# Optimization experiments

Hardware: AMD Instinct MI355X
Metric: run time of the kernel (lower is better)

## Reference

```python
import jax, jax.numpy as jnp
import numpy as np

B, S, E, NH = 1, 2048, 1024, 8
DH = E // NH
EPS_BACKEND = 1e-6  # eps in parallel_stabilized_simple
EPS_NORM = 1e-5     # MultiHeadLayerNorm (group_norm) eps


def setup_inputs() -> dict:
    key = jax.random.key(0)
    ks = jax.random.split(key, 8)
    q = jax.random.normal(ks[0], (B, S, E), jnp.float32)
    k = jax.random.normal(ks[1], (B, S, E), jnp.float32)
    v = jax.random.normal(ks[2], (B, S, E), jnp.float32)
    # gate Linear params: weight (NH, 3E), bias (NH). Small scale so gates are
    # in a realistic regime (fgate bias ~ linspace(3,6) per the torch init).
    igate_w = jax.random.normal(ks[3], (NH, 3 * E), jnp.float32) * 0.02
    igate_b = jax.random.normal(ks[4], (NH,), jnp.float32) * 0.1
    fgate_w = jax.random.normal(ks[5], (NH, 3 * E), jnp.float32) * 0.02
    fgate_b = jnp.linspace(3.0, 6.0, NH).astype(jnp.float32)
    norm_w = 1.0 + 0.1 * jax.random.normal(ks[6], (E,), jnp.float32)
    return dict(q=q, k=k, v=v, igate_w=igate_w, igate_b=igate_b,
                fgate_w=fgate_w, fgate_b=fgate_b, norm_w=norm_w)


def reference(q, k, v, igate_w, igate_b, fgate_w, fgate_b, norm_w):
    Bq, Sq, Eq = q.shape
    nh = igate_w.shape[0]
    dh = Eq // nh
    # gate pre-activations from concatenated q,k,v
    gate_in = jnp.concatenate([q, k, v], axis=-1)             # (B,S,3E)
    ig = jnp.transpose(gate_in @ igate_w.T + igate_b, (0, 2, 1))  # (B,NH,S)
    fg = jnp.transpose(gate_in @ fgate_w.T + fgate_b, (0, 2, 1))  # (B,NH,S)
    # split heads: (B,NH,S,DH)
    qh = q.reshape(Bq, Sq, nh, dh).transpose(0, 2, 1, 3)
    kh = k.reshape(Bq, Sq, nh, dh).transpose(0, 2, 1, 3)
    vh = v.reshape(Bq, Sq, nh, dh).transpose(0, 2, 1, 3)
    # cumulative log forget gates; decay matrix entry (t,s) = cs[t]-cs[s]
    log_f_cum = jnp.cumsum(jax.nn.log_sigmoid(fg), axis=-1)   # (B,NH,S)
    log_fg_mat = log_f_cum[:, :, :, None] - log_f_cum[:, :, None, :]  # (B,NH,S,S)
    ltr = jnp.tril(jnp.ones((Sq, Sq), dtype=bool))            # causal mask
    log_D = jnp.where(ltr, log_fg_mat + ig[:, :, None, :], -jnp.inf)
    # row-wise stabilizer
    max_log_D = jnp.max(log_D, axis=-1, keepdims=True)        # (B,NH,S,1)
    D = jnp.exp(log_D - max_log_D)
    qk = jnp.einsum('bhsd,bhtd->bhst', qh, kh) / jnp.sqrt(jnp.float32(dh))
    C = qk * D
    normalizer = jnp.maximum(jnp.abs(jnp.sum(C, axis=-1, keepdims=True)),
                             jnp.exp(-max_log_D))
    h = jnp.einsum('bhst,bhtd->bhsd', C / (normalizer + EPS_BACKEND), vh)
    # MultiHeadLayerNorm == group_norm with NH groups over (NH*DH), per-channel weight
    mean = jnp.mean(h, axis=-1, keepdims=True)
    var = jnp.var(h, axis=-1, keepdims=True)
    h_norm = (h - mean) / jnp.sqrt(var + EPS_NORM)
    h_norm = h_norm * norm_w.reshape(nh, dh)[None, :, None, :]
    return h_norm.transpose(0, 2, 1, 3).reshape(Bq, Sq, Eq)
```

## Files before the change

### kernel.cpp

```cpp
#include <hip/hip_runtime.h>
#include <hip/hip_bf16.h>
#include <math.h>

#define S_LEN 2048
#define E_DIM 1024
#define NHEAD 8
#define DH 128
#define E3 3072

typedef short bf16x8 __attribute__((ext_vector_type(8)));
typedef short bf16x4 __attribute__((ext_vector_type(4)));
typedef float f32x4 __attribute__((ext_vector_type(4)));
typedef float f32x16 __attribute__((ext_vector_type(16)));

#define MFMA3216(a,b,c) __builtin_amdgcn_mfma_f32_32x32x16_bf16(a,b,c,0,0,0)
#define Z16 {0.f,0.f,0.f,0.f,0.f,0.f,0.f,0.f,0.f,0.f,0.f,0.f,0.f,0.f,0.f,0.f}
#define CROW(r) (((r)&3) + 8*((r)>>2))

__device__ __forceinline__ unsigned short f2bf(float f){
  union{float f; unsigned u;} x; x.f = f;
  unsigned r = x.u + 0x7FFF + ((x.u>>16)&1);
  return (unsigned short)(r>>16);
}

__device__ __forceinline__ unsigned cvtpk(float lo, float hi){
  unsigned r;
  asm("v_cvt_pk_bf16_f32 %0, %1, %2" : "=v"(r) : "v"(lo), "v"(hi));
  return r;
}

__device__ __forceinline__ float logsigf(float x){
  return fminf(x, 0.f) - log1pf(expf(-fabsf(x)));
}

typedef const __attribute__((address_space(1))) unsigned int* gas1_t;
typedef __attribute__((address_space(3))) unsigned int* las3_t;
__device__ __forceinline__ void stage16(const ushort* g, ushort* l){
  __builtin_amdgcn_global_load_lds((gas1_t)(const void*)g, (las3_t)(void*)l, 16, 0, 0);
}

__global__ __launch_bounds__(256) void gates_qk(
    const float* __restrict__ q, const float* __restrict__ k, const float* __restrict__ v,
    const float* __restrict__ igw, const float* __restrict__ igb,
    const float* __restrict__ fgw, const float* __restrict__ fgb,
    float* __restrict__ ig_out, float* __restrict__ lsf_out,
    ushort* __restrict__ qbo, ushort* __restrict__ kbo, ushort* __restrict__ vto){
  const int t0 = blockIdx.x*4;
  const int tid = threadIdx.x;
  const int lane = tid & 63, wv = tid >> 6;
  float acc[64];
  #pragma unroll
  for (int a=0;a<64;++a) acc[a]=0.f;
  const float sc = 0.08838834764831845f;
  #pragma unroll
  for (int step=0; step<3; ++step){
    const float* src = (step==0)? q : ((step==1)? k : v);
    float4 in4[4];
    #pragma unroll
    for (int r=0;r<4;++r) in4[r] = ((const float4*)src)[(size_t)(t0+r)*256 + tid];
    if (step==0){
      #pragma unroll
      for (int r=0;r<4;++r){
        ushort4 o; o.x=f2bf(in4[r].x*sc); o.y=f2bf(in4[r].y*sc);
        o.z=f2bf(in4[r].z*sc); o.w=f2bf(in4[r].w*sc);
        ((ushort4*)qbo)[(size_t)(t0+r)*256 + tid] = o;
      }
    } else if (step==1){
      #pragma unroll
      for (int r=0;r<4;++r){
        ushort4 o; o.x=f2bf(in4[r].x); o.y=f2bf(in4[r].y);
        o.z=f2bf(in4[r].z); o.w=f2bf(in4[r].w);
        ((ushort4*)kbo)[(size_t)(t0+r)*256 + tid] = o;
      }
    } else {
      #pragma unroll
      for (int c=0;c<4;++c){
        ushort4 ov;
        ov.x = f2bf(((const float*)&in4[0])[c]);
        ov.y = f2bf(((const float*)&in4[1])[c]);
        ov.z = f2bf(((const float*)&in4[2])[c]);
        ov.w = f2bf(((const float*)&in4[3])[c]);
        *(ushort4*)(vto + (size_t)(tid*4+c)*S_LEN + t0) = ov;
      }
    }
    const int wj = step*256 + tid;
    #pragma unroll
    for (int o=0;o<8;++o){
      float4 wI = ((const float4*)igw)[o*768 + wj];
      float4 wF = ((const float4*)fgw)[o*768 + wj];
      #pragma unroll
      for (int r=0;r<4;++r){
        acc[o*4+r]    = fmaf(in4[r].x, wI.x, acc[o*4+r]);
        acc[o*4+r]    = fmaf(in4[r].y, wI.y, acc[o*4+r]);
        acc[o*4+r]    = fmaf(in4[r].z, wI.z, acc[o*4+r]);
        acc[o*4+r]    = fmaf(in4[r].w, wI.w, acc[o*4+r]);
        acc[32+o*4+r] = fmaf(in4[r].x, wF.x, acc[32+o*4+r]);
        acc[32+o*4+r] = fmaf(in4[r].y, wF.y, acc[32+o*4+r]);
        acc[32+o*4+r] = fmaf(in4[r].z, wF.z, acc[32+o*4+r]);
        acc[32+o*4+r] = fmaf(in4[r].w, wF.w, acc[32+o*4+r]);
      }
    }
  }
  int cnt = 32;
  #pragma unroll
  for (int s=0; s<6; ++s){
    const bool hib = (lane >> s) & 1;
    #pragma unroll
    for (int a=0; a<32; ++a){
      if (a < cnt){
        float sent = hib ? acc[a] : acc[a+cnt];
        float got = __shfl_xor(sent, 1<<s, 64);
        acc[a] = (hib ? acc[a+cnt] : acc[a]) + got;
      }
    }
    cnt >>= 1;
  }
  __shared__ float red[4][64];
  red[wv][lane] = acc[0];
  __syncthreads();
  if (tid < 64){
    float tot = red[0][tid]+red[1][tid]+red[2][tid]+red[3][tid];
    int a = (int)(__brev((unsigned)tid) >> 26);
    int f = a >> 5, o = (a>>2)&7, r = a&3;
    int t = t0 + r;
    if (f==0) ig_out[o*S_LEN + t] = tot + igb[o];
    else      lsf_out[o*S_LEN + t] = logsigf(tot + fgb[o]);
  }
}

__global__ __launch_bounds__(256) void scan_kernel(
    const float* __restrict__ ig, const float* __restrict__ lsf,
    float* __restrict__ cs_out, float* __restrict__ M_out, float* __restrict__ m_out){
  const int h = blockIdx.x;
  const int tid = threadIdx.x;
  __shared__ float tt[256];
  const int base = tid*8;
  const float* src = lsf + h*S_LEN;
  float loc[8]; float tot = 0.f;
  #pragma unroll
  for (int i=0;i<8;++i){ tot += src[base+i]; loc[i]=tot; }
  tt[tid]=tot; __syncthreads();
  for (int off=1; off<256; off<<=1){
    float add = (tid>=off)? tt[tid-off] : 0.f;
    __syncthreads();
    tt[tid] += add;
    __syncthreads();
  }
  const float excl = tt[tid] - tot;
  float csv[8];
  #pragma unroll
  for (int i=0;i<8;++i){ csv[i] = excl + loc[i]; cs_out[h*S_LEN+base+i]=csv[i]; }
  const float* igp = ig + h*S_LEN;
  float mloc[8], mval[8]; float mtot = -INFINITY;
  #pragma unroll
  for (int i=0;i<8;++i){
    float m = igp[base+i] - csv[i];
    mval[i] = m;
    mtot = fmaxf(mtot, m);
    mloc[i] = mtot;
  }
  __syncthreads();
  tt[tid]=mtot; __syncthreads();
  for (int off=1; off<256; off<<=1){
    float add = (tid>=off)? tt[tid-off] : -INFINITY;
    __syncthreads();
    tt[tid] = fmaxf(tt[tid], add);
    __syncthreads();
  }
  const float exclm = (tid>0)? tt[tid-1] : -INFINITY;
  #pragma unroll
  for (int i=0;i<8;++i){
    M_out[h*S_LEN+base+i] = fmaxf(exclm, mloc[i]);
    m_out[h*S_LEN+base+i] = mval[i];
  }
}

__global__ __launch_bounds__(256, 2) void mlstm_mfma6(
    const ushort* __restrict__ qb, const ushort* __restrict__ kb,
    const ushort* __restrict__ vt,
    const float* __restrict__ csb, const float* __restrict__ Mxb,
    const float* __restrict__ mbb,
    const float* __restrict__ nw, float* __restrict__ out){
  const int h = blockIdx.x;
  const int qt = 63 - blockIdx.y;
  const int tid = threadIdx.x, l = tid & 63;
  const int sq = tid >> 6;
  const int l31 = l & 31, l15 = l & 15, hi = l >> 5;

  __shared__ __align__(16) float UNI[4*32*132];
  __shared__ float MB[128];
  __shared__ float rsL[4][32];
  ushort* Kb = (ushort*)UNI;
  ushort* Vb = Kb + 16384;
  float*  Part = UNI;

  const int hS = h*S_LEN;
  const ushort* kbh = kb + h*DH;
  const ushort* vth = vt + (size_t)h*DH*S_LEN;
  const float*  mh  = mbb + hS;
  const int t0 = qt*32;
  const int NT = (t0 + 31)/128 + 1;
  const int tgq = t0 + l31;
  const float Mq = Mxb[hS + tgq];

  bf16x8 qf0,qf1,qf2,qf3,qf4,qf5,qf6,qf7;
  { const ushort* qs = qb + (size_t)tgq*E_DIM + h*DH + hi*8;
    qf0 = *(const bf16x8*)(qs+0);   qf1 = *(const bf16x8*)(qs+16);
    qf2 = *(const bf16x8*)(qs+32);  qf3 = *(const bf16x8*)(qs+48);
    qf4 = *(const bf16x8*)(qs+64);  qf5 = *(const bf16x8*)(qs+80);
    qf6 = *(const bf16x8*)(qs+96);  qf7 = *(const bf16x8*)(qs+112); }

  f32x16 a0 = Z16, a1 = Z16, a2 = Z16, a3 = Z16;
  float rsq = 0.f;

#define STAGE6(ktv) {                                                        \
    _Pragma("unroll")                                                        \
    for (int i_=0;i_<8;++i_){                                                \
      const int L_ = tid + i_*256; const int row_ = L_>>4, pc_ = L_&15;      \
      stage16(kbh + (size_t)((ktv)*128+row_)*E_DIM + ((pc_^(row_&15))<<3),   \
              Kb + (size_t)L_*8); }                                          \
    _Pragma("unroll")                                                        \
    for (int i_=0;i_<8;++i_){                                                \
      const int L_ = tid + i_*256; const int d_ = L_>>4, pc_ = L_&15;        \
      stage16(vth + (size_t)d_*S_LEN + (ktv)*128 + ((pc_^(d_&15))<<3),       \
              Vb + (size_t)L_*8); }                                          \
    if (tid < 32)                                                            \
      stage16((const ushort*)(mh + (ktv)*128) + tid*8,                       \
              (ushort*)MB + tid*8); }

#define LV6(dt, cs) (*(const bf16x8*)(Vb + (size_t)((dt)*32+l31)*128 + (((cs)^l15)<<3)))

  for (int kt=0; kt<NT; ++kt){
    if (kt) __syncthreads();
    STAGE6(kt);
    __syncthreads();

    const ushort* kbase = Kb + (size_t)(sq*32 + l31)*128;
    f32x16 cc = Z16;
    { bf16x8 ka;
      ka = *(const bf16x8*)(kbase + (((0*2+hi)^l15)<<3)); cc = MFMA3216(ka, qf0, cc);
      ka = *(const bf16x8*)(kbase + (((1*2+hi)^l15)<<3)); cc = MFMA3216(ka, qf1, cc);
      ka = *(const bf16x8*)(kbase + (((2*2+hi)^l15)<<3)); cc = MFMA3216(ka, qf2, cc);
      ka = *(const bf16x8*)(kbase + (((3*2+hi)^l15)<<3)); cc = MFMA3216(ka, qf3, cc);
      ka = *(const bf16x8*)(kbase + (((4*2+hi)^l15)<<3)); cc = MFMA3216(ka, qf4, cc);
      ka = *(const bf16x8*)(kbase + (((5*2+hi)^l15)<<3)); cc = MFMA3216(ka, qf5, cc);
      ka = *(const bf16x8*)(kbase + (((6*2+hi)^l15)<<3)); cc = MFMA3216(ka, qf6, cc);
      ka = *(const bf16x8*)(kbase + (((7*2+hi)^l15)<<3)); cc = MFMA3216(ka, qf7, cc); }

    bf16x8 fE, fO;
    {
      const int sb_ = kt*128 + sq*32 + 4*hi;
      const f32x4 mA_ = *(const f32x4*)&MB[sq*32 +  0 + 4*hi];
      const f32x4 mB_ = *(const f32x4*)&MB[sq*32 +  8 + 4*hi];
      const f32x4 mC_ = *(const f32x4*)&MB[sq*32 + 16 + 4*hi];
      const f32x4 mD_ = *(const f32x4*)&MB[sq*32 + 24 + 4*hi];
      float p0  = (sb_+0  <= tgq) ? cc[0] *__expf(mA_[0]-Mq) : 0.f;
      float p1  = (sb_+1  <= tgq) ? cc[1] *__expf(mA_[1]-Mq) : 0.f;
      float p2  = (sb_+2  <= tgq) ? cc[2] *__expf(mA_[2]-Mq) : 0.f;
      float p3  = (sb_+3  <= tgq) ? cc[3] *__expf(mA_[3]-Mq) : 0.f;
      float p4  = (sb_+8  <= tgq) ? cc[4] *__expf(mB_[0]-Mq) : 0.f;
      float p5  = (sb_+9  <= tgq) ? cc[5] *__expf(mB_[1]-Mq) : 0.f;
      float p6  = (sb_+10 <= tgq) ? cc[6] *__expf(mB_[2]-Mq) : 0.f;
      float p7  = (sb_+11 <= tgq) ? cc[7] *__expf(mB_[3]-Mq) : 0.f;
      float p8  = (sb_+16 <= tgq) ? cc[8] *__expf(mC_[0]-Mq) : 0.f;
      float p9  = (sb_+17 <= tgq) ? cc[9] *__expf(mC_[1]-Mq) : 0.f;
      float p10 = (sb_+18 <= tgq) ? cc[10]*__expf(mC_[2]-Mq) : 0.f;
      float p11 = (sb_+19 <= tgq) ? cc[11]*__expf(mC_[3]-Mq) : 0.f;
      float p12 = (sb_+24 <= tgq) ? cc[12]*__expf(mD_[0]-Mq) : 0.f;
      float p13 = (sb_+25 <= tgq) ? cc[13]*__expf(mD_[1]-Mq) : 0.f;
      float p14 = (sb_+26 <= tgq) ? cc[14]*__expf(mD_[2]-Mq) : 0.f;
      float p15 = (sb_+27 <= tgq) ? cc[15]*__expf(mD_[3]-Mq) : 0.f;
      rsq += ((p0+p1)+(p2+p3))+((p4+p5)+(p6+p7))
           + ((p8+p9)+(p10+p11))+((p12+p13)+(p14+p15));
      unsigned A0_=cvtpk(p0,p1),  A1_=cvtpk(p2,p3);
      unsigned B0_=cvtpk(p4,p5),  B1_=cvtpk(p6,p7);
      unsigned C0_=cvtpk(p8,p9),  C1_=cvtpk(p10,p11);
      unsigned D0_=cvtpk(p12,p13),D1_=cvtpk(p14,p15);
      unsigned A0x_=(unsigned)__shfl_xor((int)A0_,32,64);
      unsigned B0x_=(unsigned)__shfl_xor((int)B0_,32,64);
      unsigned A1x_=(unsigned)__shfl_xor((int)A1_,32,64);
      unsigned B1x_=(unsigned)__shfl_xor((int)B1_,32,64);
      unsigned C0x_=(unsigned)__shfl_xor((int)C0_,32,64);
      unsigned D0x_=(unsigned)__shfl_xor((int)D0_,32,64);
      unsigned C1x_=(unsigned)__shfl_xor((int)C1_,32,64);
      unsigned D1x_=(unsigned)__shfl_xor((int)D1_,32,64);
      { unsigned* u_ = (unsigned*)&fE;
        u_[0] = hi ? B0x_ : A0_;  u_[1] = hi ? B1x_ : A1_;
        u_[2] = hi ? B0_  : A0x_; u_[3] = hi ? B1_  : A1x_; }
      { unsigned* u_ = (unsigned*)&fO;
        u_[0] = hi ? D0x_ : C0_;  u_[1] = hi ? D1x_ : C1_;
        u_[2] = hi ? D0_  : C0x_; u_[3] = hi ? D1_  : C1x_; }
    }

    a0 = MFMA3216(fE, LV6(0, sq*4 + 0 + hi), a0);
    a1 = MFMA3216(fE, LV6(1, sq*4 + 0 + hi), a1);
    a2 = MFMA3216(fE, LV6(2, sq*4 + 0 + hi), a2);
    a3 = MFMA3216(fE, LV6(3, sq*4 + 0 + hi), a3);
    a0 = MFMA3216(fO, LV6(0, sq*4 + 2 + hi), a0);
    a1 = MFMA3216(fO, LV6(1, sq*4 + 2 + hi), a1);
    a2 = MFMA3216(fO, LV6(2, sq*4 + 2 + hi), a2);
    a3 = MFMA3216(fO, LV6(3, sq*4 + 2 + hi), a3);
  }

  __syncthreads();
  #pragma unroll
  for (int r=0;r<16;++r){
    const int qrow = CROW(r) + 4*hi;
    float* pr = Part + (size_t)(sq*32 + qrow)*132 + l31;
    pr[0]  = a0[r];
    pr[32] = a1[r];
    pr[64] = a2[r];
    pr[96] = a3[r];
  }
  rsq += __shfl_xor(rsq, 32, 64);
  if (l < 32) rsL[sq][l31] = rsq;
  __syncthreads();

  {
    const int q = tid >> 3, dg = tid & 7;
    f32x4 os0={0.f,0.f,0.f,0.f}, os1=os0, os2=os0, os3=os0;
    #pragma unroll
    for (int w2=0; w2<4; ++w2){
      const float* pb = Part + (size_t)(w2*32 + q)*132 + dg*16;
      os0 += *(const f32x4*)(pb+0);
      os1 += *(const f32x4*)(pb+4);
      os2 += *(const f32x4*)(pb+8);
      os3 += *(const f32x4*)(pb+12);
    }
    const float rstot = rsL[0][q]+rsL[1][q]+rsL[2][q]+rsL[3][q];
    const int tq = t0 + q;
    const float en = __expf(-(csb[hS+tq] + Mxb[hS+tq]));
    const float iv = 1.f/(fmaxf(fabsf(rstot), en) + 1e-6f);
    f32x4 h0, h1, h2, h3;
    h0[0]=os0[0]*iv; h0[1]=os0[1]*iv; h0[2]=os0[2]*iv; h0[3]=os0[3]*iv;
    h1[0]=os1[0]*iv; h1[1]=os1[1]*iv; h1[2]=os1[2]*iv; h1[3]=os1[3]*iv;
    h2[0]=os2[0]*iv; h2[1]=os2[1]*iv; h2[2]=os2[2]*iv; h2[3]=os2[3]*iv;
    h3[0]=os3[0]*iv; h3[1]=os3[1]*iv; h3[2]=os3[2]*iv; h3[3]=os3[3]*iv;
    float s1 = (h0[0]+h0[1]+h0[2]+h0[3]) + (h1[0]+h1[1]+h1[2]+h1[3])
             + (h2[0]+h2[1]+h2[2]+h2[3]) + (h3[0]+h3[1]+h3[2]+h3[3]);
    float s2 = (h0[0]*h0[0]+h0[1]*h0[1]+h0[2]*h0[2]+h0[3]*h0[3])
             + (h1[0]*h1[0]+h1[1]*h1[1]+h1[2]*h1[2]+h1[3]*h1[3])
             + (h2[0]*h2[0]+h2[1]*h2[1]+h2[2]*h2[2]+h2[3]*h2[3])
             + (h3[0]*h3[0]+h3[1]*h3[1]+h3[2]*h3[2]+h3[3]*h3[3]);
    s1 += __shfl_xor(s1, 1, 64);  s2 += __shfl_xor(s2, 1, 64);
    s1 += __shfl_xor(s1, 2, 64);  s2 += __shfl_xor(s2, 2, 64);
    s1 += __shfl_xor(s1, 4, 64);  s2 += __shfl_xor(s2, 4, 64);
    const float mean = s1*(1.f/128.f);
    const float var  = s2*(1.f/128.f) - mean*mean;
    const float rstd = rsqrtf(var + 1e-5f);
    const float* nb = nw + h*DH + dg*16;
    const f32x4 n0 = *(const f32x4*)(nb+0);
    const f32x4 n1 = *(const f32x4*)(nb+4);
    const f32x4 n2 = *(const f32x4*)(nb+8);
    const f32x4 n3 = *(const f32x4*)(nb+12);
    float* ob = out + (size_t)tq*E_DIM + h*DH + dg*16;
    f32x4 o0v, o1v, o2v, o3v;
    o0v[0]=(h0[0]-mean)*rstd*n0[0]; o0v[1]=(h0[1]-mean)*rstd*n0[1];
    o0v[2]=(h0[2]-mean)*rstd*n0[2]; o0v[3]=(h0[3]-mean)*rstd*n0[3];
    o1v[0]=(h1[0]-mean)*rstd*n1[0]; o1v[1]=(h1[1]-mean)*rstd*n1[1];
    o1v[2]=(h1[2]-mean)*rstd*n1[2]; o1v[3]=(h1[3]-mean)*rstd*n1[3];
    o2v[0]=(h2[0]-mean)*rstd*n2[0]; o2v[1]=(h2[1]-mean)*rstd*n2[1];
    o2v[2]=(h2[2]-mean)*rstd*n2[2]; o2v[3]=(h2[3]-mean)*rstd*n2[3];
    o3v[0]=(h3[0]-mean)*rstd*n3[0]; o3v[1]=(h3[1]-mean)*rstd*n3[1];
    o3v[2]=(h3[2]-mean)*rstd*n3[2]; o3v[3]=(h3[3]-mean)*rstd*n3[3];
    *(f32x4*)(ob+0)  = o0v;
    *(f32x4*)(ob+4)  = o1v;
    *(f32x4*)(ob+8)  = o2v;
    *(f32x4*)(ob+12) = o3v;
  }
}

extern "C" void kernel_launch(void* const* d_in, const int* in_sizes, int n_in,
                              void* d_out, int out_size, void* d_ws, size_t ws_size,
                              hipStream_t stream) {
  const float* q   = (const float*)d_in[0];
  const float* k   = (const float*)d_in[1];
  const float* v   = (const float*)d_in[2];
  const float* igw = (const float*)d_in[3];
  const float* igb = (const float*)d_in[4];
  const float* fgw = (const float*)d_in[5];
  const float* fgb = (const float*)d_in[6];
  const float* nw  = (const float*)d_in[7];
  float* outp = (float*)d_out;

  float* ws  = (float*)d_ws;
  float* ig  = ws;
  float* lsf = ws + 1*NHEAD*S_LEN;
  float* csb = ws + 2*NHEAD*S_LEN;
  float* Mb  = ws + 3*NHEAD*S_LEN;
  float* mbf = ws + 4*NHEAD*S_LEN;
  ushort* qbb = (ushort*)(ws + 5*NHEAD*S_LEN);
  ushort* kbb = qbb + (size_t)S_LEN*E_DIM;
  ushort* vtb = kbb + (size_t)S_LEN*E_DIM;

  gates_qk<<<S_LEN/4, 256, 0, stream>>>(q, k, v, igw, igb, fgw, fgb,
                                        ig, lsf, qbb, kbb, vtb);
  scan_kernel<<<NHEAD, 256, 0, stream>>>(ig, lsf, csb, Mb, mbf);
  mlstm_mfma6<<<dim3(NHEAD, 64), 256, 0, stream>>>(qbb, kbb, vtb, csb, Mb, mbf, nw, outp);
}
```

Measured before the change: 61.39 us.

## Halve key tile and split warps across key and head-dim halves

The key/value tile shrinks from 128 to 64 keys. The four warps are regrouped as two key halves times two head-dimension halves, so each warp accumulates only 2 PV output fragments instead of 4. Staging of the next tile is issued after the compute barrier, and the cross-warp partial reduction now combines 2 partials instead of 4, which lowers shared memory. In exchange, both head-dim warps recompute the same QK scores and exponentials, so QK MFMA and exp work per key doubles, and the kernel runs twice as many loop iterations and barriers.

```diff
diff --git a/kernel.cpp b/kernel.cpp
--- a/kernel.cpp
+++ b/kernel.cpp
@@ -175,7 +175,7 @@
   }
 }
 
-__global__ __launch_bounds__(256, 2) void mlstm_mfma6(
+__global__ __launch_bounds__(256, 2) void mlstm_mfma10(
     const ushort* __restrict__ qb, const ushort* __restrict__ kb,
     const ushort* __restrict__ vt,
     const float* __restrict__ csb, const float* __restrict__ Mxb,
@@ -187,19 +187,19 @@
   const int sq = tid >> 6;
   const int l31 = l & 31, l15 = l & 15, hi = l >> 5;
 
-  __shared__ __align__(16) float UNI[4*32*132];
-  __shared__ float MB[128];
+  __shared__ __align__(16) float UNI[8448];
   __shared__ float rsL[4][32];
   ushort* Kb = (ushort*)UNI;
-  ushort* Vb = Kb + 16384;
-  float*  Part = UNI;
+  ushort* Vb = Kb + 8192;
+  float*  MBp = UNI + 8192;
+  float*  Part2 = UNI;
 
   const int hS = h*S_LEN;
   const ushort* kbh = kb + h*DH;
   const ushort* vth = vt + (size_t)h*DH*S_LEN;
   const float*  mh  = mbb + hS;
   const int t0 = qt*32;
-  const int NT = (t0 + 31)/128 + 1;
+  const int NT = (t0 + 31)/64 + 1;
   const int tgq = t0 + l31;
   const float Mq = Mxb[hS + tgq];
 
@@ -213,121 +213,137 @@
   f32x16 a0 = Z16, a1 = Z16, a2 = Z16, a3 = Z16;
   float rsq = 0.f;
 
-#define STAGE6(ktv) {                                                        \
+#define STAGE10(ktv) {                                                       \
     _Pragma("unroll")                                                        \
-    for (int i_=0;i_<8;++i_){                                                \
+    for (int i_=0;i_<4;++i_){                                                \
       const int L_ = tid + i_*256; const int row_ = L_>>4, pc_ = L_&15;      \
-      stage16(kbh + (size_t)((ktv)*128+row_)*E_DIM + ((pc_^(row_&15))<<3),   \
+      stage16(kbh + (size_t)((ktv)*64+row_)*E_DIM + ((pc_^(row_&15))<<3),    \
               Kb + (size_t)L_*8); }                                          \
     _Pragma("unroll")                                                        \
-    for (int i_=0;i_<8;++i_){                                                \
-      const int L_ = tid + i_*256; const int d_ = L_>>4, pc_ = L_&15;        \
-      stage16(vth + (size_t)d_*S_LEN + (ktv)*128 + ((pc_^(d_&15))<<3),       \
+    for (int i_=0;i_<4;++i_){                                                \
+      const int L_ = tid + i_*256; const int d_ = L_>>3, pc_ = L_&7;         \
+      stage16(vth + (size_t)d_*S_LEN + (ktv)*64 + ((pc_^(d_&7))<<3),         \
               Vb + (size_t)L_*8); }                                          \
-    if (tid < 32)                                                            \
-      stage16((const ushort*)(mh + (ktv)*128) + tid*8,                       \
-              (ushort*)MB + tid*8); }
-
-#define LV6(dt, cs) (*(const bf16x8*)(Vb + (size_t)((dt)*32+l31)*128 + (((cs)^l15)<<3)))
-
+    if (tid < 16)                                                            \
+      stage16((const ushort*)(mh + (ktv)*64) + tid*8,                        \
+              (ushort*)MBp + tid*8); }
+
+  const int sh = sq & 1;
+  const int dh2 = sq >> 1;
+
+  STAGE10(0);
   for (int kt=0; kt<NT; ++kt){
     if (kt) __syncthreads();
-    STAGE6(kt);
+    else    __syncthreads();
+    if (false) {}
+    {
+      const ushort* kbase = Kb + (size_t)(sh*32 + l31)*128;
+      f32x16 cc = Z16;
+      { bf16x8 ka;
+        ka = *(const bf16x8*)(kbase + (((0*2+hi)^l15)<<3)); cc = MFMA3216(ka, qf0, cc);
+        ka = *(const bf16x8*)(kbase + (((1*2+hi)^l15)<<3)); cc = MFMA3216(ka, qf1, cc);
+        ka = *(const bf16x8*)(kbase + (((2*2+hi)^l15)<<3)); cc = MFMA3216(ka, qf2, cc);
+        ka = *(const bf16x8*)(kbase + (((3*2+hi)^l15)<<3)); cc = MFMA3216(ka, qf3, cc);
+        ka = *(const bf16x8*)(kbase + (((4*2+hi)^l15)<<3)); cc = MFMA3216(ka, qf4, cc);
+        ka = *(const bf16x8*)(kbase + (((5*2+hi)^l15)<<3)); cc = MFMA3216(ka, qf5, cc);
+        ka = *(const bf16x8*)(kbase + (((6*2+hi)^l15)<<3)); cc = MFMA3216(ka, qf6, cc);
+        ka = *(const bf16x8*)(kbase + (((7*2+hi)^l15)<<3)); cc = MFMA3216(ka, qf7, cc); }
+
+      bf16x8 fE, fO;
+      {
+        const int sb_ = kt*64 + sh*32 + 4*hi;
+        const f32x4 mA_ = *(const f32x4*)&MBp[sh*32 +  0 + 4*hi];
+        const f32x4 mB_ = *(const f32x4*)&MBp[sh*32 +  8 + 4*hi];
+        const f32x4 mC_ = *(const f32x4*)&MBp[sh*32 + 16 + 4*hi];
+        const f32x4 mD_ = *(const f32x4*)&MBp[sh*32 + 24 + 4*hi];
+        float p0  = (sb_+0  <= tgq) ? cc[0] *__expf(mA_[0]-Mq) : 0.f;
+        float p1  = (sb_+1  <= tgq) ? cc[1] *__expf(mA_[1]-Mq) : 0.f;
+        float p2  = (sb_+2  <= tgq) ? cc[2] *__expf(mA_[2]-Mq) : 0.f;
+        float p3  = (sb_+3  <= tgq) ? cc[3] *__expf(mA_[3]-Mq) : 0.f;
+        float p4  = (sb_+8  <= tgq) ? cc[4] *__expf(mB_[0]-Mq) : 0.f;
+        float p5  = (sb_+9  <= tgq) ? cc[5] *__expf(mB_[1]-Mq) : 0.f;
+        float p6  = (sb_+10 <= tgq) ? cc[6] *__expf(mB_[2]-Mq) : 0.f;
+        float p7  = (sb_+11 <= tgq) ? cc[7] *__expf(mB_[3]-Mq) : 0.f;
+        float p8  = (sb_+16 <= tgq) ? cc[8] *__expf(mC_[0]-Mq) : 0.f;
+        float p9  = (sb_+17 <= tgq) ? cc[9] *__expf(mC_[1]-Mq) : 0.f;
+        float p10 = (sb_+18 <= tgq) ? cc[10]*__expf(mC_[2]-Mq) : 0.f;
+        float p11 = (sb_+19 <= tgq) ? cc[11]*__expf(mC_[3]-Mq) : 0.f;
+        float p12 = (sb_+24 <= tgq) ? cc[12]*__expf(mD_[0]-Mq) : 0.f;
+        float p13 = (sb_+25 <= tgq) ? cc[13]*__expf(mD_[1]-Mq) : 0.f;
+        float p14 = (sb_+26 <= tgq) ? cc[14]*__expf(mD_[2]-Mq) : 0.f;
+        float p15 = (sb_+27 <= tgq) ? cc[15]*__expf(mD_[3]-Mq) : 0.f;
+        if (dh2 == 0)
+          rsq += ((p0+p1)+(p2+p3))+((p4+p5)+(p6+p7))
+               + ((p8+p9)+(p10+p11))+((p12+p13)+(p14+p15));
+        unsigned A0_=cvtpk(p0,p1),  A1_=cvtpk(p2,p3);
+        unsigned B0_=cvtpk(p4,p5),  B1_=cvtpk(p6,p7);
+        unsigned C0_=cvtpk(p8,p9),  C1_=cvtpk(p10,p11);
+        unsigned D0_=cvtpk(p12,p13),D1_=cvtpk(p14,p15);
+        unsigned A0x_=(unsigned)__shfl_xor((int)A0_,32,64);
+        unsigned B0x_=(unsigned)__shfl_xor((int)B0_,32,64);
+        unsigned A1x_=(unsigned)__shfl_xor((int)A1_,32,64);
+        unsigned B1x_=(unsigned)__shfl_xor((int)B1_,32,64);
+        unsigned C0x_=(unsigned)__shfl_xor((int)C0_,32,64);
+        unsigned D0x_=(unsigned)__shfl_xor((int)D0_,32,64);
+        unsigned C1x_=(unsigned)__shfl_xor((int)C1_,32,64);
+        unsigned D1x_=(unsigned)__shfl_xor((int)D1_,32,64);
+        { unsigned* u_ = (unsigned*)&fE;
+          u_[0] = hi ? B0x_ : A0_;  u_[1] = hi ? B1x_ : A1_;
+          u_[2] = hi ? B0_  : A0x_; u_[3] = hi ? B1_  : A1x_; }
+        { unsigned* u_ = (unsigned*)&fO;
+          u_[0] = hi ? D0x_ : C0_;  u_[1] = hi ? D1x_ : C1_;
+          u_[2] = hi ? D0_  : C0x_; u_[3] = hi ? D1_  : C1x_; }
+      }
+
+#define LV10(dt, cs) (*(const bf16x8*)(Vb + (size_t)((dh2*2+(dt))*32+l31)*64 + (((cs)^((((dh2*2+(dt))*32+l31)&7)))<<3)))
+      a0 = MFMA3216(fE, LV10(0, sh*4 + 0 + hi), a0);
+      a1 = MFMA3216(fE, LV10(1, sh*4 + 0 + hi), a1);
+      a0 = MFMA3216(fO, LV10(0, sh*4 + 2 + hi), a0);
+      a1 = MFMA3216(fO, LV10(1, sh*4 + 2 + hi), a1);
+#undef LV10
+    }
     __syncthreads();
-
-    const ushort* kbase = Kb + (size_t)(sq*32 + l31)*128;
-    f32x16 cc = Z16;
-    { bf16x8 ka;
-      ka = *(const bf16x8*)(kbase + (((0*2+hi)^l15)<<3)); cc = MFMA3216(ka, qf0, cc);
-      ka = *(const bf16x8*)(kbase + (((1*2+hi)^l15)<<3)); cc = MFMA3216(ka, qf1, cc);
-      ka = *(const bf16x8*)(kbase + (((2*2+hi)^l15)<<3)); cc = MFMA3216(ka, qf2, cc);
-      ka = *(const bf16x8*)(kbase + (((3*2+hi)^l15)<<3)); cc = MFMA3216(ka, qf3, cc);
-      ka = *(const bf16x8*)(kbase + (((4*2+hi)^l15)<<3)); cc = MFMA3216(ka, qf4, cc);
-      ka = *(const bf16x8*)(kbase + (((5*2+hi)^l15)<<3)); cc = MFMA3216(ka, qf5, cc);
-      ka = *(const bf16x8*)(kbase + (((6*2+hi)^l15)<<3)); cc = MFMA3216(ka, qf6, cc);
-      ka = *(const bf16x8*)(kbase + (((7*2+hi)^l15)<<3)); cc = MFMA3216(ka, qf7, cc); }
-
-    bf16x8 fE, fO;
-    {
-      const int sb_ = kt*128 + sq*32 + 4*hi;
-      const f32x4 mA_ = *(const f32x4*)&MB[sq*32 +  0 + 4*hi];
-      const f32x4 mB_ = *(const f32x4*)&MB[sq*32 +  8 + 4*hi];
-      const f32x4 mC_ = *(const f32x4*)&MB[sq*32 + 16 + 4*hi];
-      const f32x4 mD_ = *(const f32x4*)&MB[sq*32 + 24 + 4*hi];
-      float p0  = (sb_+0  <= tgq) ? cc[0] *__expf(mA_[0]-Mq) : 0.f;
-      float p1  = (sb_+1  <= tgq) ? cc[1] *__expf(mA_[1]-Mq) : 0.f;
-      float p2  = (sb_+2  <= tgq) ? cc[2] *__expf(mA_[2]-Mq) : 0.f;
-      float p3  = (sb_+3  <= tgq) ? cc[3] *__expf(mA_[3]-Mq) : 0.f;
-      float p4  = (sb_+8  <= tgq) ? cc[4] *__expf(mB_[0]-Mq) : 0.f;
-      float p5  = (sb_+9  <= tgq) ? cc[5] *__expf(mB_[1]-Mq) : 0.f;
-      float p6  = (sb_+10 <= tgq) ? cc[6] *__expf(mB_[2]-Mq) : 0.f;
-      float p7  = (sb_+11 <= tgq) ? cc[7] *__expf(mB_[3]-Mq) : 0.f;
-      float p8  = (sb_+16 <= tgq) ? cc[8] *__expf(mC_[0]-Mq) : 0.f;
-      float p9  = (sb_+17 <= tgq) ? cc[9] *__expf(mC_[1]-Mq) : 0.f;
-      float p10 = (sb_+18 <= tgq) ? cc[10]*__expf(mC_[2]-Mq) : 0.f;
-      float p11 = (sb_+19 <= tgq) ? cc[11]*__expf(mC_[3]-Mq) : 0.f;
-      float p12 = (sb_+24 <= tgq) ? cc[12]*__expf(mD_[0]-Mq) : 0.f;
-      float p13 = (sb_+25 <= tgq) ? cc[13]*__expf(mD_[1]-Mq) : 0.f;
-      float p14 = (sb_+26 <= tgq) ? cc[14]*__expf(mD_[2]-Mq) : 0.f;
-      float p15 = (sb_+27 <= tgq) ? cc[15]*__expf(mD_[3]-Mq) : 0.f;
-      rsq += ((p0+p1)+(p2+p3))+((p4+p5)+(p6+p7))
-           + ((p8+p9)+(p10+p11))+((p12+p13)+(p14+p15));
-      unsigned A0_=cvtpk(p0,p1),  A1_=cvtpk(p2,p3);
-      unsigned B0_=cvtpk(p4,p5),  B1_=cvtpk(p6,p7);
-      unsigned C0_=cvtpk(p8,p9),  C1_=cvtpk(p10,p11);
-      unsigned D0_=cvtpk(p12,p13),D1_=cvtpk(p14,p15);
-      unsigned A0x_=(unsigned)__shfl_xor((int)A0_,32,64);
-      unsigned B0x_=(unsigned)__shfl_xor((int)B0_,32,64);
-      unsigned A1x_=(unsigned)__shfl_xor((int)A1_,32,64);
-      unsigned B1x_=(unsigned)__shfl_xor((int)B1_,32,64);
-      unsigned C0x_=(unsigned)__shfl_xor((int)C0_,32,64);
-      unsigned D0x_=(unsigned)__shfl_xor((int)D0_,32,64);
-      unsigned C1x_=(unsigned)__shfl_xor((int)C1_,32,64);
-      unsigned D1x_=(unsigned)__shfl_xor((int)D1_,32,64);
-      { unsigned* u_ = (unsigned*)&fE;
-        u_[0] = hi ? B0x_ : A0_;  u_[1] = hi ? B1x_ : A1_;
-        u_[2] = hi ? B0_  : A0x_; u_[3] = hi ? B1_  : A1x_; }
-      { unsigned* u_ = (unsigned*)&fO;
-        u_[0] = hi ? D0x_ : C0_;  u_[1] = hi ? D1x_ : C1_;
-        u_[2] = hi ? D0_  : C0x_; u_[3] = hi ? D1_  : C1x_; }
-    }
-
-    a0 = MFMA3216(fE, LV6(0, sq*4 + 0 + hi), a0);
-    a1 = MFMA3216(fE, LV6(1, sq*4 + 0 + hi), a1);
-    a2 = MFMA3216(fE, LV6(2, sq*4 + 0 + hi), a2);
-    a3 = MFMA3216(fE, LV6(3, sq*4 + 0 + hi), a3);
-    a0 = MFMA3216(fO, LV6(0, sq*4 + 2 + hi), a0);
-    a1 = MFMA3216(fO, LV6(1, sq*4 + 2 + hi), a1);
-    a2 = MFMA3216(fO, LV6(2, sq*4 + 2 + hi), a2);
-    a3 = MFMA3216(fO, LV6(3, sq*4 + 2 + hi), a3);
+    if (kt+1 < NT){ STAGE10(kt+1); }
   }
 
   __syncthreads();
-  #pragma unroll
-  for (int r=0;r<16;++r){
-    const int qrow = CROW(r) + 4*hi;
-    float* pr = Part + (size_t)(sq*32 + qrow)*132 + l31;
-    pr[0]  = a0[r];
-    pr[32] = a1[r];
-    pr[64] = a2[r];
-    pr[96] = a3[r];
+  if (sq < 2){
+    #pragma unroll
+    for (int r=0;r<16;++r){
+      const int qrow = CROW(r) + 4*hi;
+      float* pr = Part2 + (size_t)(sh*32 + qrow)*132 + l31;
+      pr[0]  = a0[r];
+      pr[32] = a1[r];
+      pr[64] = 0.f;
+      pr[96] = 0.f;
+    }
   }
   rsq += __shfl_xor(rsq, 32, 64);
   if (l < 32) rsL[sq][l31] = rsq;
   __syncthreads();
+  if (sq >= 2){
+    #pragma unroll
+    for (int r=0;r<16;++r){
+      const int qrow = CROW(r) + 4*hi;
+      float* pr = Part2 + (size_t)(sh*32 + qrow)*132 + l31;
+      pr[64] = a0[r];
+      pr[96] = a1[r];
+    }
+  }
+  __syncthreads();
 
   {
     const int q = tid >> 3, dg = tid & 7;
     f32x4 os0={0.f,0.f,0.f,0.f}, os1=os0, os2=os0, os3=os0;
     #pragma unroll
-    for (int w2=0; w2<4; ++w2){
-      const float* pb = Part + (size_t)(w2*32 + q)*132 + dg*16;
+    for (int w2=0; w2<2; ++w2){
+      const float* pb = Part2 + (size_t)(w2*32 + q)*132 + dg*16;
       os0 += *(const f32x4*)(pb+0);
       os1 += *(const f32x4*)(pb+4);
       os2 += *(const f32x4*)(pb+8);
       os3 += *(const f32x4*)(pb+12);
     }
-    const float rstot = rsL[0][q]+rsL[1][q]+rsL[2][q]+rsL[3][q];
+    const float rstot = rsL[0][q]+rsL[1][q];
     const int tq = t0 + q;
     const float en = __expf(-(csb[hS+tq] + Mxb[hS+tq]));
     const float iv = 1.f/(fmaxf(fabsf(rstot), en) + 1e-6f);
@@ -396,5 +412,5 @@
   gates_qk<<<S_LEN/4, 256, 0, stream>>>(q, k, v, igw, igb, fgw, fgb,
                                         ig, lsf, qbb, kbb, vtb);
   scan_kernel<<<NHEAD, 256, 0, stream>>>(ig, lsf, csb, Mb, mbf);
-  mlstm_mfma6<<<dim3(NHEAD, 64), 256, 0, stream>>>(qbb, kbb, vtb, csb, Mb, mbf, nw, outp);
-}
+  mlstm_mfma10<<<dim3(NHEAD, 64), 256, 0, stream>>>(qbb, kbb, vtb, csb, Mb, mbf, nw, outp);
+}
```

New measurement: 74.10 us. +20.7%, slower.
